# Kernel optimization log

Measured on AMD Instinct MI355X. Metric: run time of the kernel, lower is better.

Reference implementation:

```python
import jax, jax.numpy as jnp
import numpy as np

# Water box constants: n_atoms=192 -> 64 oxygens (type 8) + 128 hydrogens (type 1)
N_O, N_H = 64, 128
XLIM = 6.0  # params.max_rdf_dist


def _hist(d, bins):
    """np.histogram-equivalent fixed-bin histogram of 1-D values d."""
    nb = bins.shape[0] - 1
    idx = jnp.clip(jnp.searchsorted(bins, d, side='right') - 1, 0, nb - 1)
    w = ((d >= bins[0]) & (d <= bins[-1])).astype(jnp.float32)
    return jnp.zeros((nb,), jnp.float32).at[idx].add(w)


def _pair_rdf(wrapped, idx0, idx1, lattices, bins):
    # wrapped: [T, N, 3]; replicates distance_pbc_select + histogram/RDF math
    x0 = wrapped[:, idx0]                       # [T, n0, 3] (type1 atoms)
    x1 = wrapped[:, idx1]                       # [T, n1, 3] (type2 atoms)
    # x0.repeat([1,n1,1]) vs x1.repeat_interleave(n0) == outer pairing (x1 outer, x0 inner)
    delta = jnp.abs(x0[:, None, :, :] - x1[:, :, None, :])   # [T, n1, n0, 3]
    delta = jnp.where(delta > 0.5 * lattices, delta - lattices, delta)
    s = (delta ** 2).sum(-1)                    # [T, n1, n0]
    # safe sqrt (self-pairs give exact zeros)
    d = jnp.where(s > 0, jnp.sqrt(jnp.where(s > 0, s, 1.0)), 0.0)
    T = d.shape[0]
    P = d.shape[1] * d.shape[2]
    d = d.reshape(T, P)
    hists = jax.vmap(lambda dd: _hist(dd, bins))(d)          # [T, nb]
    vol = jnp.prod(lattices)
    shell = (4.0 / 3.0) * jnp.pi * (bins[1:] ** 3 - bins[:-1] ** 3)
    # aggregate RDF over all frames (zeros fall below bins[0]=1e-6, excluded)
    Z1 = (T * P / vol) * shell
    data_rdf = hists.sum(0) / Z1
    # per-frame RDFs, renormalized to the aggregate RDF's total mass
    Z2 = (T / vol) * shell
    rdfs = hists / Z2
    rdfs = rdfs / rdfs.sum(1, keepdims=True) * data_rdf.sum()
    return rdfs.mean(0)                          # [nb]


def setup_inputs() -> dict:
    key = jax.random.key(0)
    k0, k1, k2, k3 = jax.random.split(key, 4)
    T, R, N, nb = 100, 8, 192, 600
    stacked_radii = jax.random.normal(k0, (T, R, N, 3), jnp.float32) * 5.0
    ptypes = jnp.tile(jnp.array([8, 1, 1], jnp.int32), N // 3)  # O,H,H per water
    lattices = jnp.full((3,), 12.42, jnp.float32)
    bins = jnp.asarray(np.linspace(1e-6, XLIM, nb + 1), jnp.float32)
    gt_oo = jax.random.uniform(k1, (1, nb), jnp.float32)
    gt_hh = jax.random.uniform(k2, (1, nb), jnp.float32)
    gt_ho = jax.random.uniform(k3, (1, nb), jnp.float32)
    return dict(stacked_radii=stacked_radii, ptypes=ptypes, lattices=lattices,
                bins=bins, gt_oo=gt_oo, gt_hh=gt_hh, gt_ho=gt_ho)


def reference(stacked_radii, ptypes, lattices, bins, gt_oo, gt_hh, gt_ho):
    idx_O = jnp.nonzero(ptypes == 8, size=N_O)[0]
    idx_H = jnp.nonzero(ptypes == 1, size=N_H)[0]

    def per_replica(data):                       # data: [T, N, 3]
        wrapped = data / lattices % 1 * lattices  # PBC wrap into box
        rdf_oo = _pair_rdf(wrapped, idx_O, idx_O, lattices, bins)
        rdf_hh = _pair_rdf(wrapped, idx_H, idx_H, lattices, bins)
        rdf_ho = _pair_rdf(wrapped, idx_H, idx_O, lattices, bins)
        maes = jnp.stack([
            XLIM * jnp.abs(rdf_oo[None] - gt_oo).mean(),
            XLIM * jnp.abs(rdf_hh[None] - gt_hh).mean(),
            XLIM * jnp.abs(rdf_ho[None] - gt_ho).mean(),
        ])
        return jnp.concatenate([rdf_oo, rdf_hh, rdf_ho]), maes.max()

    # [T, R, N, 3] -> [R, T, N, 3], vmap over replicas
    rdf_list, max_maes = jax.vmap(per_replica)(jnp.swapaxes(stacked_radii, 0, 1))
    return rdf_list, max_maes
```

## Files before the change

### kernel.cpp

```cpp
#include <hip/hip_runtime.h>

#define T_STEPS 100
#define R_REP   8
#define N_ATOMS 192
#define NBINS   600

__global__ __launch_bounds__(256) void rdf_hist_kernel(
    const float* __restrict__ radii,
    const float* __restrict__ lattices,
    const float* __restrict__ bins,
    float* __restrict__ hist_out,
    float* __restrict__ sigma_out)
{
#pragma clang fp contract(off)
    __shared__ float    sbins[NBINS + 1];
    __shared__ unsigned shist[4][NBINS];
    __shared__ float4   sA[128];
    __shared__ float4   sB[64];
    __shared__ float    sred[256];

    const int blk = blockIdx.x;
    const int p   = blk % 3;
    const int t   = (blk / 3) % T_STEPS;
    const int r   = blk / (3 * T_STEPS);
    const int tid = threadIdx.x;

    for (int b = tid; b <= NBINS; b += 256) sbins[b] = bins[b];
    for (int b = tid; b < NBINS; b += 256) {
        shist[0][b] = 0u; shist[1][b] = 0u; shist[2][b] = 0u; shist[3][b] = 0u;
    }

    const float L0 = lattices[0], L1 = lattices[1], L2 = lattices[2];
    const float* base = radii + (size_t)(t * R_REP + r) * (N_ATOMS * 3);

    auto load_set = [&](float4* dst, int n, bool isH) {
#pragma clang fp contract(off)
        for (int a = tid; a < n; a += 256) {
            int atom = isH ? (3 * (a >> 1) + 1 + (a & 1)) : (3 * a);
            const float* src = base + atom * 3;
            float x = src[0], y = src[1], z = src[2];
            float qx = x / L0; float wx = (qx - floorf(qx)) * L0;
            float qy = y / L1; float wy = (qy - floorf(qy)) * L1;
            float qz = z / L2; float wz = (qz - floorf(qz)) * L2;
            dst[a] = make_float4(wx, wy, wz, 0.0f);
        }
    };

    if (p == 0)      { load_set(sA, 64, false); }
    else if (p == 1) { load_set(sA, 128, true); }
    else             { load_set(sA, 128, true); load_set(sB, 64, false); }
    __syncthreads();

    const float b0 = sbins[0], bN = sbins[NBINS];
    const float invstep = (float)NBINS / (bN - b0);
    const float sCut = bN * bN * 1.001f;
    const float h0 = 0.5f * L0, h1 = 0.5f * L1, h2 = 0.5f * L2;
    unsigned* myh = shist[tid >> 6];

    auto bin_pair = [&](float4 A, float4 B, unsigned w) {
#pragma clang fp contract(off)
        float dx = fabsf(A.x - B.x); if (dx > h0) dx = dx - L0;
        float dy = fabsf(A.y - B.y); if (dy > h1) dy = dy - L1;
        float dz = fabsf(A.z - B.z); if (dz > h2) dz = dz - L2;
        float s = dx * dx + dy * dy + dz * dz;
        if (s <= 0.0f || s > sCut) return;
        float d = sqrtf(s);
        if (d < b0 || d > bN) return;
        int k0 = (int)((d - b0) * invstep);
        if (k0 > NBINS - 1) k0 = NBINS - 1;
        float lo = sbins[k0], hi = sbins[k0 + 1];
        int bi = k0 + (int)(d >= hi) - (int)(d < lo);
        if (bi > NBINS - 1) bi = NBINS - 1;
        atomicAdd(&myh[bi], w);
    };

    if (p == 2) {
        for (int it = 0; it < 32; ++it) {
            int q = tid + it * 256;
            bin_pair(sA[q & 127], sB[q >> 7], 1u);
        }
    } else if (p == 1) {
        for (int it = 0; it < 32; ++it) {
            int q = tid + it * 256;
            int i = q & 127;
            int k = (q >> 7) + 1;
            int j = (i + k) & 127;
            bin_pair(sA[i], sA[j], (k == 64) ? 1u : 2u);
        }
    } else {
        for (int it = 0; it < 8; ++it) {
            int q = tid + it * 256;
            int i = q & 63;
            int k = (q >> 6) + 1;
            int j = (i + k) & 63;
            bin_pair(sA[i], sA[j], (k == 32) ? 1u : 2u);
        }
    }
    __syncthreads();

    float* outp = hist_out + (size_t)((r * 3 + p) * T_STEPS + t) * NBINS;
    float lsig = 0.0f;
    for (int b = tid; b < NBINS; b += 256) {
        float fc = (float)(shist[0][b] + shist[1][b] + shist[2][b] + shist[3][b]);
        outp[b] = fc;
        float e0 = sbins[b], e1 = sbins[b + 1];
        float shell = 4.18879020478639053f * (e1 * e1 * e1 - e0 * e0 * e0);
        lsig += fc / shell;
    }
    sred[tid] = lsig;
    __syncthreads();
    for (int s2 = 128; s2 > 0; s2 >>= 1) {
        if (tid < s2) sred[tid] += sred[tid + s2];
        __syncthreads();
    }
    if (tid == 0) sigma_out[(r * 3 + p) * T_STEPS + t] = sred[0];
}

__global__ __launch_bounds__(640) void rdf_norm_kernel(
    const float* __restrict__ hist,
    const float* __restrict__ sigma,
    const float* __restrict__ bins,
    const float* __restrict__ lattices,
    const float* __restrict__ gt_oo,
    const float* __restrict__ gt_hh,
    const float* __restrict__ gt_ho,
    float* __restrict__ out)
{
#pragma clang fp contract(off)
    __shared__ float ssig[T_STEPS];
    __shared__ float sinvsig[T_STEPS];
    __shared__ float sred[640];
    __shared__ float sS;

    const int blk = blockIdx.x;
    const int p = blk % 3, r = blk / 3;
    const int tid = threadIdx.x;
    const float* h = hist + (size_t)blk * T_STEPS * NBINS;

    if (tid < T_STEPS) {
        float sg = sigma[blk * T_STEPS + tid];
        ssig[tid] = sg;
        sinvsig[tid] = 1.0f / sg;
    }
    __syncthreads();
    if (tid == 0) {
        float s = 0.0f;
        for (int t = 0; t < T_STEPS; ++t) s += ssig[t];
        float vol = lattices[0] * lattices[1] * lattices[2];
        float Pf = (p == 0) ? 4096.0f : ((p == 1) ? 16384.0f : 8192.0f);
        sS = vol / ((float)T_STEPS * Pf) * s;
    }
    __syncthreads();

    const float S = sS;
    const float* gt = (p == 0) ? gt_oo : ((p == 1) ? gt_hh : gt_ho);
    float lacc = 0.0f;
    const int b = tid;
    if (b < NBINS) {
        float a0 = 0.0f, a1 = 0.0f, a2 = 0.0f, a3 = 0.0f;
        const float* hb = h + b;
        for (int t = 0; t < T_STEPS; t += 4) {
            a0 += hb[(t + 0) * NBINS] * sinvsig[t + 0];
            a1 += hb[(t + 1) * NBINS] * sinvsig[t + 1];
            a2 += hb[(t + 2) * NBINS] * sinvsig[t + 2];
            a3 += hb[(t + 3) * NBINS] * sinvsig[t + 3];
        }
        float e0 = bins[b], e1 = bins[b + 1];
        float shell = 4.18879020478639053f * (e1 * e1 * e1 - e0 * e0 * e0);
        float v = S * (1.0f / (float)T_STEPS) * (1.0f / shell) * ((a0 + a1) + (a2 + a3));
        out[r * 1800 + p * 600 + b] = v;
        lacc = fabsf(v - gt[b]);
    }
    sred[tid] = lacc;
    __syncthreads();
    for (int s2 = 512; s2 > 0; s2 >>= 1) {
        if (tid < s2 && tid + s2 < 640) sred[tid] += sred[tid + s2];
        __syncthreads();
    }
    if (tid == 0) {
        float mae = 6.0f * (sred[0] / 600.0f);
        atomicMax((int*)&out[14400 + r], __float_as_int(mae));
    }
}

extern "C" void kernel_launch(void* const* d_in, const int* in_sizes, int n_in,
                              void* d_out, int out_size, void* d_ws, size_t ws_size,
                              hipStream_t stream) {
    const float* radii    = (const float*)d_in[0];
    const float* lattices = (const float*)d_in[2];
    const float* bins     = (const float*)d_in[3];
    const float* gt_oo    = (const float*)d_in[4];
    const float* gt_hh    = (const float*)d_in[5];
    const float* gt_ho    = (const float*)d_in[6];
    float* out = (float*)d_out;

    float* hist  = (float*)d_ws;
    float* sigma = hist + (size_t)R_REP * 3 * T_STEPS * NBINS;

    hipLaunchKernelGGL(rdf_hist_kernel, dim3(R_REP * 3 * T_STEPS), dim3(256), 0, stream,
                       radii, lattices, bins, hist, sigma);
    hipLaunchKernelGGL(rdf_norm_kernel, dim3(R_REP * 3), dim3(640), 0, stream,
                       hist, sigma, bins, lattices, gt_oo, gt_hh, gt_ho, out);
}
```

Measured before the change: 97.58 us.

## Bin by squared distance against precomputed squared thresholds, hoist per-thread atom loads

Precomputes, per bin edge, the smallest float whose sqrt reaches that edge. Binning can then compare the squared distance instead of needing an IEEE-exact sqrt, and a fast hardware sqrt only picks the approximate bin. The minimum-image wrap becomes branch-free fminf, and the pair loops are restructured so each thread keeps its A atom in a register and fully unrolls over partners. The cost is extra per-block setup running bit-search loops over 601 edges, a hardcoded 6.0 upper edge, and reliance on the threshold table matching sqrt rounding exactly.

```diff
diff --git a/kernel.cpp b/kernel.cpp
--- a/kernel.cpp
+++ b/kernel.cpp
@@ -13,7 +13,7 @@
     float* __restrict__ sigma_out)
 {
 #pragma clang fp contract(off)
-    __shared__ float    sbins[NBINS + 1];
+    __shared__ float    Tq[NBINS + 2];
     __shared__ unsigned shist[4][NBINS];
     __shared__ float4   sA[128];
     __shared__ float4   sB[64];
@@ -25,7 +25,20 @@
     const int r   = blk / (3 * T_STEPS);
     const int tid = threadIdx.x;
 
-    for (int b = tid; b <= NBINS; b += 256) sbins[b] = bins[b];
+    for (int b = tid; b <= NBINS + 1; b += 256) {
+        if (b <= NBINS) {
+            float e = bins[b];
+            unsigned u = __float_as_uint(e * e);
+            while (sqrtf(__uint_as_float(u)) <  e) ++u;
+            while (sqrtf(__uint_as_float(u - 1)) >= e) --u;
+            Tq[b] = __uint_as_float(u);
+        } else {
+            unsigned u = __float_as_uint(36.0f);
+            while (sqrtf(__uint_as_float(u)) <= 6.0f) ++u;
+            while (sqrtf(__uint_as_float(u - 1)) > 6.0f) --u;
+            Tq[NBINS + 1] = __uint_as_float(u);
+        }
+    }
     for (int b = tid; b < NBINS; b += 256) {
         shist[0][b] = 0u; shist[1][b] = 0u; shist[2][b] = 0u; shist[3][b] = 0u;
     }
@@ -51,49 +64,52 @@
     else             { load_set(sA, 128, true); load_set(sB, 64, false); }
     __syncthreads();
 
-    const float b0 = sbins[0], bN = sbins[NBINS];
-    const float invstep = (float)NBINS / (bN - b0);
-    const float sCut = bN * bN * 1.001f;
+    const float T0 = Tq[0];
+    const float TG = Tq[NBINS + 1];
+    const float b0f = bins[0];
+    const float invstep = (float)NBINS / (6.0f - b0f);
     const float h0 = 0.5f * L0, h1 = 0.5f * L1, h2 = 0.5f * L2;
     unsigned* myh = shist[tid >> 6];
 
     auto bin_pair = [&](float4 A, float4 B, unsigned w) {
 #pragma clang fp contract(off)
-        float dx = fabsf(A.x - B.x); if (dx > h0) dx = dx - L0;
-        float dy = fabsf(A.y - B.y); if (dy > h1) dy = dy - L1;
-        float dz = fabsf(A.z - B.z); if (dz > h2) dz = dz - L2;
+        float dx = fabsf(A.x - B.x); dx = fminf(dx, fabsf(dx - L0));
+        float dy = fabsf(A.y - B.y); dy = fminf(dy, fabsf(dy - L1));
+        float dz = fabsf(A.z - B.z); dz = fminf(dz, fabsf(dz - L2));
         float s = dx * dx + dy * dy + dz * dz;
-        if (s <= 0.0f || s > sCut) return;
-        float d = sqrtf(s);
-        if (d < b0 || d > bN) return;
-        int k0 = (int)((d - b0) * invstep);
+        if (s < T0 || s >= TG) return;
+        float dhat = __builtin_amdgcn_sqrtf(s);
+        int k0 = (int)((dhat - b0f) * invstep);
         if (k0 > NBINS - 1) k0 = NBINS - 1;
-        float lo = sbins[k0], hi = sbins[k0 + 1];
-        int bi = k0 + (int)(d >= hi) - (int)(d < lo);
+        float lo = Tq[k0], hi = Tq[k0 + 1];
+        int bi = k0 + (int)(s >= hi) - (int)(s < lo);
         if (bi > NBINS - 1) bi = NBINS - 1;
         atomicAdd(&myh[bi], w);
     };
 
     if (p == 2) {
+        float4 A = sA[tid & 127];
+        int jbase = (tid >> 7);
+#pragma unroll
+        for (int it = 0; it < 32; ++it)
+            bin_pair(A, sB[jbase + it * 2], 1u);
+    } else if (p == 1) {
+        int i = tid & 127;
+        float4 A = sA[i];
+        int kbase = (tid >> 7) + 1;
+#pragma unroll
         for (int it = 0; it < 32; ++it) {
-            int q = tid + it * 256;
-            bin_pair(sA[q & 127], sB[q >> 7], 1u);
-        }
-    } else if (p == 1) {
-        for (int it = 0; it < 32; ++it) {
-            int q = tid + it * 256;
-            int i = q & 127;
-            int k = (q >> 7) + 1;
-            int j = (i + k) & 127;
-            bin_pair(sA[i], sA[j], (k == 64) ? 1u : 2u);
+            int k = kbase + it * 2;
+            bin_pair(A, sA[(i + k) & 127], (k == 64) ? 1u : 2u);
         }
     } else {
+        int i = tid & 63;
+        float4 A = sA[i];
+        int kbase = (tid >> 6) + 1;
+#pragma unroll
         for (int it = 0; it < 8; ++it) {
-            int q = tid + it * 256;
-            int i = q & 63;
-            int k = (q >> 6) + 1;
-            int j = (i + k) & 63;
-            bin_pair(sA[i], sA[j], (k == 32) ? 1u : 2u);
+            int k = kbase + it * 4;
+            bin_pair(A, sA[(i + k) & 63], (k == 32) ? 1u : 2u);
         }
     }
     __syncthreads();
@@ -103,7 +119,7 @@
     for (int b = tid; b < NBINS; b += 256) {
         float fc = (float)(shist[0][b] + shist[1][b] + shist[2][b] + shist[3][b]);
         outp[b] = fc;
-        float e0 = sbins[b], e1 = sbins[b + 1];
+        float e0 = bins[b], e1 = bins[b + 1];
         float shell = 4.18879020478639053f * (e1 * e1 * e1 - e0 * e0 * e0);
         lsig += fc / shell;
     }
```

New measurement: 92.38 us. 5.3% less time.
